# Kernel tuning notes

Hardware: AMD Instinct MI355X
Metric: run time of the kernel (lower is better)

Reference implementation:

```python
import jax, jax.numpy as jnp
import numpy as np

WS = 7            # small window size
WU = 14           # big window size (2*WS)
DIM = 192
HEADS = 6
HD = DIM // HEADS
HID = int(DIM * 4.0)

def _rel_index():
    bc = np.stack(np.meshgrid(np.arange(WU), np.arange(WU), indexing='ij')).reshape(2, -1)
    sc = np.stack(np.meshgrid(np.arange(WS), np.arange(WS), indexing='ij')).reshape(2, -1)
    rc = (bc[:, :, None] - sc[:, None, :]).transpose(1, 2, 0).astype(np.int64)  # [196,49,2]
    rc[..., 0] += WU - 1
    rc[..., 1] += WU - 1
    rc[..., 0] *= 2 * WU - 1
    return rc.sum(-1)  # [196,49]

REL_IDX = jnp.asarray(_rel_index())

def _layernorm(x, w, b):
    mu = x.mean(-1, keepdims=True)
    var = ((x - mu) ** 2).mean(-1, keepdims=True)
    return (x - mu) * jax.lax.rsqrt(var + 1e-5) * w + b

def _partition(x, ws):
    # x: (B,H,W,C) -> (B*nW, ws*ws, C)
    B, H, W, C = x.shape
    x = x.reshape(B, H // ws, ws, W // ws, ws, C).transpose(0, 1, 3, 2, 4, 5)
    return x.reshape(-1, ws * ws, C)

def _reverse(win, ws, B, H, W):
    C = win.shape[-1]
    x = win.reshape(B, H // ws, W // ws, ws, ws, C).transpose(0, 1, 3, 2, 4, 5)
    return x.reshape(B, H, W, C)

def setup_inputs() -> dict:
    key = jax.random.key(0)
    ks = jax.random.split(key, 12)
    s = 0.02
    return {
        'big_x': jax.random.normal(ks[0], (2, DIM, 224, 224), jnp.float32),
        'small_x': jax.random.normal(ks[1], (2, DIM, 112, 112), jnp.float32),
        'norm_w': jnp.ones((DIM,), jnp.float32),
        'norm_b': jnp.zeros((DIM,), jnp.float32),
        'qkv_w': jax.random.normal(ks[2], (DIM, 3 * DIM), jnp.float32) * s,
        'qkv_b': jnp.zeros((3 * DIM,), jnp.float32),
        'rpb_table': jax.random.normal(ks[3], ((2 * WU - 1) ** 2, HEADS), jnp.float32) * s,
        'proj_w': jax.random.normal(ks[4], (DIM, DIM), jnp.float32) * s,
        'proj_b': jnp.zeros((DIM,), jnp.float32),
        'fc1_w': jax.random.normal(ks[5], (DIM, HID), jnp.float32) * s,
        'fc1_b': jnp.zeros((HID,), jnp.float32),
        'fc2_w': jax.random.normal(ks[6], (HID, DIM), jnp.float32) * s,
        'fc2_b': jnp.zeros((DIM,), jnp.float32),
    }

def reference(big_x, small_x, norm_w, norm_b, qkv_w, qkv_b, rpb_table,
              proj_w, proj_b, fc1_w, fc1_b, fc2_w, fc2_b):
    B, C, Hb, Wb = big_x.shape
    shortcut = big_x.transpose(0, 2, 3, 1)              # B,H,W,C
    bx = _layernorm(shortcut, norm_w, norm_b)
    sx = _layernorm(small_x.transpose(0, 2, 3, 1), norm_w, norm_b)

    xb = _partition(bx, WU)                             # (Bw, 196, C)
    xs = _partition(sx, WS)                             # (Bw, 49, C)
    Bw, Nb, _ = xb.shape
    Ns = xs.shape[1]

    def qkv_split(x, N):
        q = (x @ qkv_w + qkv_b).reshape(-1, N, 3, HEADS, HD).transpose(2, 0, 3, 1, 4)
        return q[0], q[1], q[2]

    qb, _, _ = qkv_split(xb, Nb)
    _, ks_, vs = qkv_split(xs, Ns)

    # NOTE: original forward never applies self.scale -> no scaling, faithful.
    attn = jnp.einsum('bhnd,bhmd->bhnm', qb, ks_)       # (Bw,H,196,49)
    bias = rpb_table[REL_IDX]                           # (196,49,H)
    attn = jax.nn.softmax(attn + bias.transpose(2, 0, 1)[None], axis=-1)
    out = jnp.einsum('bhnm,bhmd->bhnd', attn, vs)       # (Bw,H,196,hd)
    out = out.transpose(0, 2, 1, 3).reshape(Bw, Nb, C)
    out = out @ proj_w + proj_b

    x = shortcut + _reverse(out, WU, B, Hb, Wb)
    h = _layernorm(x, norm_w, norm_b)
    h = jax.nn.gelu(h @ fc1_w + fc1_b, approximate=False) @ fc2_w + fc2_b
    x = x + h
    return x.transpose(0, 3, 1, 2)
```

## Files before the change

### kernel.cpp

```cpp
#include <hip/hip_runtime.h>
#include <hip/hip_bf16.h>

typedef __attribute__((ext_vector_type(8))) short bf16x8;
typedef __attribute__((ext_vector_type(4))) float f32x4;

__device__ __forceinline__ unsigned short f2b(float f){
  union { float f; unsigned int u; } v; v.f = f;
  unsigned int r = (v.u + 0x7FFFu + ((v.u >> 16) & 1u)) >> 16;
  return (unsigned short)r;
}
__device__ __forceinline__ float b2f(unsigned short s){
  union { unsigned int u; float f; } v; v.u = ((unsigned int)s) << 16;
  return v.f;
}
__device__ __forceinline__ f32x4 mfma16(bf16x8 a, bf16x8 b, f32x4 c){
  return __builtin_amdgcn_mfma_f32_16x16x32_bf16(a, b, c, 0, 0, 0);
}


__global__ __launch_bounds__(256) void k_wconv(const float* __restrict__ qkv_w, const float* __restrict__ proj_w,
                                               const float* __restrict__ fc1_w, const float* __restrict__ fc2_w,
                                               unsigned short* __restrict__ wT){
  int i = blockIdx.x*256 + threadIdx.x;
  if (i < 110592){
    int k = i / 576, n = i - k*576;
    wT[n*192 + k] = f2b(qkv_w[i]);
  } else if (i < 147456){
    int j = i - 110592; int k = j / 192, n = j - k*192;
    wT[110592 + n*192 + k] = f2b(proj_w[j]);
  } else if (i < 294912){
    int j = i - 147456; int k = j / 768, n = j - k*768;
    wT[147456 + n*192 + k] = f2b(fc1_w[j]);
  } else {
    int j = i - 294912; int k = j / 192, n = j - k*192;
    wT[294912 + n*768 + k] = f2b(fc2_w[j]);
  }
}

template<int IMG, int WSZ, int NTOK>
__global__ __launch_bounds__(256) void k_ln(const float* __restrict__ xin, const float* __restrict__ nw,
                                            const float* __restrict__ nb, unsigned short* __restrict__ out){
  const int HW = IMG*IMG;
  int tid = threadIdx.x;
  int p = blockIdx.x*256 + tid;
  int b = p / HW, rem = p - b*HW;
  const float* base = xin + (size_t)b*192*HW + rem;
  float s = 0.f, s2 = 0.f;
  for (int c = 0; c < 192; c++){ float v = base[(size_t)c*HW]; s += v; s2 += v*v; }
  float mu = s*(1.f/192.f);
  float var = s2*(1.f/192.f) - mu*mu;
  float rs = rsqrtf(var + 1e-5f);
  int y = rem / IMG, xx = rem - y*IMG;
  int wy = y / WSZ, iy = y - wy*WSZ, wx = xx / WSZ, ix = xx - wx*WSZ;
  int t = ((b*16 + wy)*16 + wx)*NTOK + iy*WSZ + ix;
  __shared__ int srow[256];
  __shared__ unsigned short tile[256][66];
  srow[tid] = t*192;
  int lane = tid & 63, w = tid >> 6;
  for (int c0 = 0; c0 < 192; c0 += 64){
    for (int j = 0; j < 64; j++){
      int c = c0 + j;
      float v = base[(size_t)c*HW];
      tile[tid][j] = f2b((v - mu)*rs*nw[c] + nb[c]);
    }
    __syncthreads();
    for (int i = 0; i < 64; i++){
      int pix = w*64 + i;
      out[srow[pix] + c0 + lane] = tile[pix][lane];
    }
    __syncthreads();
  }
}

__global__ __launch_bounds__(256) void k_gemm_full(const unsigned short* A, const unsigned short* Bt,
                                                   const float* __restrict__ bias, unsigned short* C, int Nstride){
  int m0 = blockIdx.x * 64;
  int nbase = blockIdx.y * 192;
  int tid = threadIdx.x, lane = tid & 63, w = tid >> 6;
  int wm = w & 1, wn = w >> 1;
  int r16 = lane & 15, g = lane >> 4, kk8 = g*8;
  __shared__ __align__(16) unsigned short Al[64][40];
  __shared__ __align__(16) unsigned short Bl[192][40];
  f32x4 acc[2][6];
  const f32x4 zz = {0.f,0.f,0.f,0.f};
  for (int a_ = 0; a_ < 2; a_++) for (int b_ = 0; b_ < 6; b_++) acc[a_][b_] = zz;
  int srow = tid >> 2, sseg = (tid & 3)*8;
  for (int k0 = 0; k0 < 192; k0 += 32){
    *(bf16x8*)&Al[srow][sseg] = *(const bf16x8*)&A[(size_t)(m0 + srow)*192 + k0 + sseg];
    for (int s = 0; s < 3; s++){
      int rr = srow + 64*s;
      *(bf16x8*)&Bl[rr][sseg] = *(const bf16x8*)&Bt[(size_t)(nbase + rr)*192 + k0 + sseg];
    }
    __syncthreads();
    bf16x8 a0 = *(bf16x8*)&Al[wm*32 + r16][kk8];
    bf16x8 a1 = *(bf16x8*)&Al[wm*32 + 16 + r16][kk8];
    for (int nj = 0; nj < 6; nj++){
      bf16x8 bb = *(bf16x8*)&Bl[wn*96 + nj*16 + r16][kk8];
      acc[0][nj] = mfma16(a0, bb, acc[0][nj]);
      acc[1][nj] = mfma16(a1, bb, acc[1][nj]);
    }
    __syncthreads();
  }
  for (int mi = 0; mi < 2; mi++) for (int nj = 0; nj < 6; nj++){
    int n = wn*96 + nj*16 + r16;
    float bv = bias[nbase + n];
    for (int r = 0; r < 4; r++){
      int m = m0 + wm*32 + mi*16 + g*4 + r;
      C[(size_t)m*Nstride + nbase + n] = f2b(acc[mi][nj][r] + bv);
    }
  }
}

__global__ __launch_bounds__(256) void k_proj_res(const unsigned short* __restrict__ A,
                                                  const unsigned short* __restrict__ Bt,
                                                  const float* __restrict__ bias,
                                                  const float* __restrict__ big, float* __restrict__ xout){
  int pix0 = blockIdx.x * 64;
  int b = pix0 / 50176, rem0 = pix0 - b*50176;
  int tid = threadIdx.x, lane = tid & 63, w = tid >> 6;
  int wm = w & 1, wn = w >> 1;
  int r16 = lane & 15, g = lane >> 4, kk8 = g*8;
  __shared__ int tok[64];
  __shared__ __align__(16) char smem[49664];
  unsigned short (*Al)[40] = (unsigned short (*)[40])smem;
  unsigned short (*Bl)[40] = (unsigned short (*)[40])(smem + 5120);
  float (*ot)[193] = (float (*)[193])smem;
  if (tid < 64){
    int rem = rem0 + tid, y = rem / 224, x = rem - y*224;
    tok[tid] = ((b*16 + y/14)*16 + x/14)*196 + (y%14)*14 + (x%14);
  }
  __syncthreads();
  int srow = tid >> 2, sseg = (tid & 3)*8;
  int myTok = tok[srow];
  f32x4 acc[2][6];
  const f32x4 zz = {0.f,0.f,0.f,0.f};
  for (int a_ = 0; a_ < 2; a_++) for (int b_ = 0; b_ < 6; b_++) acc[a_][b_] = zz;
  for (int k0 = 0; k0 < 192; k0 += 32){
    *(bf16x8*)&Al[srow][sseg] = *(const bf16x8*)&A[(size_t)myTok*192 + k0 + sseg];
    for (int s = 0; s < 3; s++){
      int rr = srow + 64*s;
      *(bf16x8*)&Bl[rr][sseg] = *(const bf16x8*)&Bt[(size_t)rr*192 + k0 + sseg];
    }
    __syncthreads();
    bf16x8 a0 = *(bf16x8*)&Al[wm*32 + r16][kk8];
    bf16x8 a1 = *(bf16x8*)&Al[wm*32 + 16 + r16][kk8];
    for (int nj = 0; nj < 6; nj++){
      bf16x8 bb = *(bf16x8*)&Bl[wn*96 + nj*16 + r16][kk8];
      acc[0][nj] = mfma16(a0, bb, acc[0][nj]);
      acc[1][nj] = mfma16(a1, bb, acc[1][nj]);
    }
    __syncthreads();
  }
  for (int mi = 0; mi < 2; mi++) for (int nj = 0; nj < 6; nj++){
    int n = wn*96 + nj*16 + r16;
    float bv = bias[n];
    for (int r = 0; r < 4; r++)
      ot[wm*32 + mi*16 + g*4 + r][n] = acc[mi][nj][r] + bv;
  }
  __syncthreads();
  for (int j = 0; j < 48; j++){
    int flat = j*256 + tid;
    int c = flat >> 6, p = flat & 63;
    size_t addr = ((size_t)b*192 + c)*50176 + rem0 + p;
    xout[addr] = ot[p][c] + big[addr];
  }
}

__global__ __launch_bounds__(256) void k_attn(unsigned short* q, const unsigned short* __restrict__ kv,
                                              const float* __restrict__ rpb){
  int win = blockIdx.x / 6, head = blockIdx.x - win*6;
  int tid = threadIdx.x, lane = tid & 63, w = tid >> 6;
  __shared__ __align__(16) unsigned short ql[208][40];
  __shared__ __align__(16) unsigned short kl[64][40];
  __shared__ __align__(16) unsigned short vt[32][72];
  __shared__ __align__(16) unsigned short plds[4][16][72];
  __shared__ float rb[729];
  float4 z4; z4.x = z4.y = z4.z = z4.w = 0.f;
  {
    float4* a4 = (float4*)&ql[0][0];
    for (int i = tid; i < 1040; i += 256) a4[i] = z4;
    float4* b4 = (float4*)&kl[0][0];
    for (int i = tid; i < 320; i += 256) b4[i] = z4;
    float4* c4 = (float4*)&vt[0][0];
    for (int i = tid; i < 288; i += 256) c4[i] = z4;
  }
  __syncthreads();
  const unsigned short* qbase = q + (size_t)win*196*192 + head*32;
  for (int r4 = tid; r4 < 784; r4 += 256){
    int r = r4 >> 2, seg = (r4 & 3)*8;
    *(bf16x8*)&ql[r][seg] = *(const bf16x8*)&qbase[(size_t)r*192 + seg];
  }
  const unsigned short* kbase = kv + (size_t)win*49*384 + head*32;
  if (tid < 196){
    int r = tid >> 2, seg = (tid & 3)*8;
    *(bf16x8*)&kl[r][seg] = *(const bf16x8*)&kbase[(size_t)r*384 + seg];
  }
  const unsigned short* vbase = kbase + 192;
  for (int md = tid; md < 392; md += 256){
    int m = md >> 3, d0 = (md & 7)*4;
    const unsigned short* src = vbase + (size_t)m*384 + d0;
    vt[d0][m] = src[0]; vt[d0+1][m] = src[1]; vt[d0+2][m] = src[2]; vt[d0+3][m] = src[3];
  }
  for (int i = tid; i < 729; i += 256) rb[i] = rpb[i*6 + head];
  __syncthreads();
  int r16 = lane & 15, g = lane >> 4, kk8 = g*8;
  const f32x4 zz = {0.f,0.f,0.f,0.f};
  unsigned short* obase = q + (size_t)win*196*192 + head*32;
  for (int mt = w; mt < 13; mt += 4){
    bf16x8 a = *(bf16x8*)&ql[mt*16 + r16][kk8];
    f32x4 s[4];
    for (int nt = 0; nt < 4; nt++){
      bf16x8 bb = *(bf16x8*)&kl[nt*16 + r16][kk8];
      s[nt] = mfma16(a, bb, zz);
    }
    int nb0 = mt*16 + g*4;
    for (int nt = 0; nt < 4; nt++){
      int m = nt*16 + r16;
      if (m < 49){
        int jy = m / 7, jx = m - jy*7;
        for (int r = 0; r < 4; r++){
          int n = nb0 + r; if (n > 195) n = 195;
          int iy = n / 14, ix = n - iy*14;
          s[nt][r] += rb[(iy - jy + 13)*27 + (ix - jx + 13)];
        }
      } else {
        s[nt][0] = -1e30f; s[nt][1] = -1e30f; s[nt][2] = -1e30f; s[nt][3] = -1e30f;
      }
    }
    for (int r = 0; r < 4; r++){
      float mx = fmaxf(fmaxf(s[0][r], s[1][r]), fmaxf(s[2][r], s[3][r]));
      mx = fmaxf(mx, __shfl_xor(mx, 1, 16));
      mx = fmaxf(mx, __shfl_xor(mx, 2, 16));
      mx = fmaxf(mx, __shfl_xor(mx, 4, 16));
      mx = fmaxf(mx, __shfl_xor(mx, 8, 16));
      float sum = 0.f;
      for (int nt = 0; nt < 4; nt++){ float e = __expf(s[nt][r] - mx); s[nt][r] = e; sum += e; }
      sum += __shfl_xor(sum, 1, 16);
      sum += __shfl_xor(sum, 2, 16);
      sum += __shfl_xor(sum, 4, 16);
      sum += __shfl_xor(sum, 8, 16);
      float inv = 1.0f / sum;
      for (int nt = 0; nt < 4; nt++) s[nt][r] *= inv;
    }
    for (int nt = 0; nt < 4; nt++)
      for (int r = 0; r < 4; r++)
        plds[w][g*4 + r][nt*16 + r16] = f2b(s[nt][r]);
    asm volatile("s_waitcnt lgkmcnt(0)" ::: "memory");
    f32x4 o0 = zz, o1 = zz;
    for (int ks = 0; ks < 2; ks++){
      bf16x8 pa = *(bf16x8*)&plds[w][r16][ks*32 + kk8];
      bf16x8 v0 = *(bf16x8*)&vt[r16][ks*32 + kk8];
      bf16x8 v1 = *(bf16x8*)&vt[16 + r16][ks*32 + kk8];
      o0 = mfma16(pa, v0, o0);
      o1 = mfma16(pa, v1, o1);
    }
    for (int r = 0; r < 4; r++){
      int n = nb0 + r;
      if (n < 196){
        obase[(size_t)n*192 + r16]      = f2b(o0[r]);
        obase[(size_t)n*192 + 16 + r16] = f2b(o1[r]);
      }
    }
  }
}

__global__ __launch_bounds__(512) void k_mlp(float* xio, const unsigned short* __restrict__ fc1T, const float* __restrict__ b1,
                                             const unsigned short* __restrict__ fc2T, const float* __restrict__ b2,
                                             const float* __restrict__ nw, const float* __restrict__ nb){
  __shared__ __align__(16) unsigned short xv[64][198];
  __shared__ __align__(16) unsigned short xln[64][200];
  __shared__ __align__(16) unsigned short ul[64][72];
  int pix0 = blockIdx.x * 64;
  int b = pix0 / 50176, rem0 = pix0 - b*50176;
  int tid = threadIdx.x, lane = tid & 63, w = tid >> 6;
  float xr[24];
  for (int i = 0; i < 24; i++){
    int c = i*8 + (tid >> 6), p = tid & 63;
    float v = xio[((size_t)b*192 + c)*50176 + rem0 + p];
    xr[i] = v;
    xv[p][c] = f2b(v);
  }
  __syncthreads();
  {
    int row = tid >> 3, sub = tid & 7;
    float s = 0.f, s2 = 0.f;
    for (int j = 0; j < 24; j++){ float v = b2f(xv[row][sub*24 + j]); s += v; s2 += v*v; }
    s  += __shfl_xor(s, 1, 8);  s2 += __shfl_xor(s2, 1, 8);
    s  += __shfl_xor(s, 2, 8);  s2 += __shfl_xor(s2, 2, 8);
    s  += __shfl_xor(s, 4, 8);  s2 += __shfl_xor(s2, 4, 8);
    float mu = s*(1.f/192.f), var = s2*(1.f/192.f) - mu*mu, rs = rsqrtf(var + 1e-5f);
    for (int j = 0; j < 24; j++){
      int c = sub*24 + j;
      float v = b2f(xv[row][c]);
      xln[row][c] = f2b((v - mu)*rs*nw[c] + nb[c]);
    }
  }
  __syncthreads();
  int wm = w >> 2, wn = w & 3;
  int r16 = lane & 15, g = lane >> 4, kk8 = g*8;
  const f32x4 zz = {0.f,0.f,0.f,0.f};
  f32x4 acc2[2][3];
  acc2[0][0]=zz; acc2[0][1]=zz; acc2[0][2]=zz; acc2[1][0]=zz; acc2[1][1]=zz; acc2[1][2]=zz;
  for (int kh = 0; kh < 12; kh++){
    f32x4 u0 = zz, u1 = zz;
    int nc = kh*64 + wn*16 + r16;
    for (int ks = 0; ks < 6; ks++){
      bf16x8 bb = *(const bf16x8*)&fc1T[(size_t)nc*192 + ks*32 + kk8];
      bf16x8 a0 = *(bf16x8*)&xln[wm*32 + r16][ks*32 + kk8];
      bf16x8 a1 = *(bf16x8*)&xln[wm*32 + 16 + r16][ks*32 + kk8];
      u0 = mfma16(a0, bb, u0);
      u1 = mfma16(a1, bb, u1);
    }
    float bias1 = b1[nc];
    for (int r = 0; r < 4; r++){
      float uu = u0[r] + bias1;
      ul[wm*32 + g*4 + r][wn*16 + r16]      = f2b(0.5f*uu*(1.f + erff(uu*0.70710678f)));
      float vv = u1[r] + bias1;
      ul[wm*32 + 16 + g*4 + r][wn*16 + r16] = f2b(0.5f*vv*(1.f + erff(vv*0.70710678f)));
    }
    __syncthreads();
    for (int ks = 0; ks < 2; ks++){
      bf16x8 a0 = *(bf16x8*)&ul[wm*32 + r16][ks*32 + kk8];
      bf16x8 a1 = *(bf16x8*)&ul[wm*32 + 16 + r16][ks*32 + kk8];
      for (int j = 0; j < 3; j++){
        int n2 = wn*16 + j*64 + r16;
        bf16x8 bb = *(const bf16x8*)&fc2T[(size_t)n2*768 + kh*64 + ks*32 + kk8];
        acc2[0][j] = mfma16(a0, bb, acc2[0][j]);
        acc2[1][j] = mfma16(a1, bb, acc2[1][j]);
      }
    }
    __syncthreads();
  }
  for (int mi = 0; mi < 2; mi++) for (int j = 0; j < 3; j++){
    int c = wn*16 + j*64 + r16;
    float bias2 = b2[c];
    for (int r = 0; r < 4; r++){
      int t = wm*32 + mi*16 + g*4 + r;
      xv[t][c] = f2b(acc2[mi][j][r] + bias2);
    }
  }
  __syncthreads();
  for (int i = 0; i < 24; i++){
    int c = i*8 + (tid >> 6), p = tid & 63;
    xio[((size_t)b*192 + c)*50176 + rem0 + p] = xr[i] + b2f(xv[p][c]);
  }
}

extern "C" void kernel_launch(void* const* d_in, const int* in_sizes, int n_in,
                              void* d_out, int out_size, void* d_ws, size_t ws_size,
                              hipStream_t stream){
  (void)in_sizes; (void)n_in; (void)out_size; (void)ws_size;
  const float* bigx   = (const float*)d_in[0];
  const float* smx    = (const float*)d_in[1];
  const float* nw     = (const float*)d_in[2];
  const float* nb_    = (const float*)d_in[3];
  const float* qkv_w  = (const float*)d_in[4];
  const float* qkv_b  = (const float*)d_in[5];
  const float* rpb    = (const float*)d_in[6];
  const float* proj_w = (const float*)d_in[7];
  const float* proj_b = (const float*)d_in[8];
  const float* fc1_w  = (const float*)d_in[9];
  const float* fc1_b  = (const float*)d_in[10];
  const float* fc2_w  = (const float*)d_in[11];
  const float* fc2_b  = (const float*)d_in[12];

  char* ws = (char*)d_ws;
  unsigned short* wT  = (unsigned short*)ws;
  unsigned short* bxn = (unsigned short*)(ws + 884736);
  unsigned short* xsn = (unsigned short*)(ws + 39419904);
  unsigned short* kvb = (unsigned short*)(ws + 49053696);
  float* xo = (float*)d_out;

  k_wconv<<<1728, 256, 0, stream>>>(qkv_w, proj_w, fc1_w, fc2_w, wT);
  k_ln<224,14,196><<<392, 256, 0, stream>>>(bigx, nw, nb_, bxn);
  k_ln<112,7,49><<<98, 256, 0, stream>>>(smx, nw, nb_, xsn);
  k_gemm_full<<<dim3(1568,1), 256, 0, stream>>>(bxn, wT, qkv_b, bxn, 192);
  k_gemm_full<<<dim3(392,2), 256, 0, stream>>>(xsn, wT + 36864, qkv_b + 192, kvb, 384);
  k_attn<<<3072, 256, 0, stream>>>(bxn, kvb, rpb);
  k_proj_res<<<1568, 256, 0, stream>>>(bxn, wT + 110592, proj_b, bigx, xo);
  k_mlp<<<1568, 512, 0, stream>>>(xo, wT + 147456, fc1_b, wT + 294912, fc2_b, nw, nb_);
}
```

Measured before the change: 684.3 us.

## Double-buffer MLP hidden chunks, drop register/LDS copies, raise occupancy

Restructures k_mlp so the next fc1+GELU chunk is computed into a second LDS buffer while the current chunk feeds fc2, removing one barrier per iteration. The fc1 K-loop is split into two independent accumulator chains for more MFMA ILP. The layernorm output overwrites the input buffer and the 24-float residual register copy is dropped, with the residual re-read from global at the end. A min-blocks hint of 5 is added to launch_bounds to lower register and LDS pressure for higher occupancy. The trade is an extra global read of x and possible register spills under the tighter bound.

```diff
diff --git a/kernel.cpp b/kernel.cpp
--- a/kernel.cpp
+++ b/kernel.cpp
@@ -264,21 +264,17 @@
   }
 }
 
-__global__ __launch_bounds__(512) void k_mlp(float* xio, const unsigned short* __restrict__ fc1T, const float* __restrict__ b1,
-                                             const unsigned short* __restrict__ fc2T, const float* __restrict__ b2,
-                                             const float* __restrict__ nw, const float* __restrict__ nb){
-  __shared__ __align__(16) unsigned short xv[64][198];
-  __shared__ __align__(16) unsigned short xln[64][200];
-  __shared__ __align__(16) unsigned short ul[64][72];
+__global__ __launch_bounds__(512, 5) void k_mlp(float* xio, const unsigned short* __restrict__ fc1T, const float* __restrict__ b1,
+                                                const unsigned short* __restrict__ fc2T, const float* __restrict__ b2,
+                                                const float* __restrict__ nw, const float* __restrict__ nb){
+  __shared__ __align__(16) unsigned short xv[64][200];
+  __shared__ __align__(16) unsigned short ul[2][64][72];
   int pix0 = blockIdx.x * 64;
   int b = pix0 / 50176, rem0 = pix0 - b*50176;
   int tid = threadIdx.x, lane = tid & 63, w = tid >> 6;
-  float xr[24];
   for (int i = 0; i < 24; i++){
     int c = i*8 + (tid >> 6), p = tid & 63;
-    float v = xio[((size_t)b*192 + c)*50176 + rem0 + p];
-    xr[i] = v;
-    xv[p][c] = f2b(v);
+    xv[p][c] = f2b(xio[((size_t)b*192 + c)*50176 + rem0 + p]);
   }
   __syncthreads();
   {
@@ -292,36 +288,47 @@
     for (int j = 0; j < 24; j++){
       int c = sub*24 + j;
       float v = b2f(xv[row][c]);
-      xln[row][c] = f2b((v - mu)*rs*nw[c] + nb[c]);
+      xv[row][c] = f2b((v - mu)*rs*nw[c] + nb[c]);
     }
   }
   __syncthreads();
   int wm = w >> 2, wn = w & 3;
   int r16 = lane & 15, g = lane >> 4, kk8 = g*8;
   const f32x4 zz = {0.f,0.f,0.f,0.f};
+
+#define FC1_CHUNK(KH, BUF)                                                          \
+  {                                                                                 \
+    f32x4 u0a = zz, u0b = zz, u1a = zz, u1b = zz;                                   \
+    int nc = (KH)*64 + wn*16 + r16;                                                 \
+    for (int ks = 0; ks < 3; ks++){                                                 \
+      bf16x8 bb0 = *(const bf16x8*)&fc1T[(size_t)nc*192 + ks*32 + kk8];             \
+      bf16x8 bb1 = *(const bf16x8*)&fc1T[(size_t)nc*192 + (ks+3)*32 + kk8];         \
+      bf16x8 a0 = *(bf16x8*)&xv[wm*32 + r16][ks*32 + kk8];                          \
+      bf16x8 a1 = *(bf16x8*)&xv[wm*32 + 16 + r16][ks*32 + kk8];                     \
+      bf16x8 a0b = *(bf16x8*)&xv[wm*32 + r16][(ks+3)*32 + kk8];                     \
+      bf16x8 a1b = *(bf16x8*)&xv[wm*32 + 16 + r16][(ks+3)*32 + kk8];                \
+      u0a = mfma16(a0, bb0, u0a);  u1a = mfma16(a1, bb0, u1a);                      \
+      u0b = mfma16(a0b, bb1, u0b); u1b = mfma16(a1b, bb1, u1b);                     \
+    }                                                                               \
+    float b1v = b1[nc];                                                             \
+    for (int r = 0; r < 4; r++){                                                    \
+      float uu = u0a[r] + u0b[r] + b1v;                                             \
+      ul[BUF][wm*32 + g*4 + r][wn*16 + r16]      = f2b(0.5f*uu*(1.f + erff(uu*0.70710678f))); \
+      float vv = u1a[r] + u1b[r] + b1v;                                             \
+      ul[BUF][wm*32 + 16 + g*4 + r][wn*16 + r16] = f2b(0.5f*vv*(1.f + erff(vv*0.70710678f))); \
+    }                                                                               \
+  }
+
   f32x4 acc2[2][3];
   acc2[0][0]=zz; acc2[0][1]=zz; acc2[0][2]=zz; acc2[1][0]=zz; acc2[1][1]=zz; acc2[1][2]=zz;
+  FC1_CHUNK(0, 0)
+  __syncthreads();
   for (int kh = 0; kh < 12; kh++){
-    f32x4 u0 = zz, u1 = zz;
-    int nc = kh*64 + wn*16 + r16;
-    for (int ks = 0; ks < 6; ks++){
-      bf16x8 bb = *(const bf16x8*)&fc1T[(size_t)nc*192 + ks*32 + kk8];
-      bf16x8 a0 = *(bf16x8*)&xln[wm*32 + r16][ks*32 + kk8];
-      bf16x8 a1 = *(bf16x8*)&xln[wm*32 + 16 + r16][ks*32 + kk8];
-      u0 = mfma16(a0, bb, u0);
-      u1 = mfma16(a1, bb, u1);
-    }
-    float bias1 = b1[nc];
-    for (int r = 0; r < 4; r++){
-      float uu = u0[r] + bias1;
-      ul[wm*32 + g*4 + r][wn*16 + r16]      = f2b(0.5f*uu*(1.f + erff(uu*0.70710678f)));
-      float vv = u1[r] + bias1;
-      ul[wm*32 + 16 + g*4 + r][wn*16 + r16] = f2b(0.5f*vv*(1.f + erff(vv*0.70710678f)));
-    }
-    __syncthreads();
+    int cur = kh & 1;
+    if (kh < 11){ FC1_CHUNK(kh+1, cur^1) }
     for (int ks = 0; ks < 2; ks++){
-      bf16x8 a0 = *(bf16x8*)&ul[wm*32 + r16][ks*32 + kk8];
-      bf16x8 a1 = *(bf16x8*)&ul[wm*32 + 16 + r16][ks*32 + kk8];
+      bf16x8 a0 = *(bf16x8*)&ul[cur][wm*32 + r16][ks*32 + kk8];
+      bf16x8 a1 = *(bf16x8*)&ul[cur][wm*32 + 16 + r16][ks*32 + kk8];
       for (int j = 0; j < 3; j++){
         int n2 = wn*16 + j*64 + r16;
         bf16x8 bb = *(const bf16x8*)&fc2T[(size_t)n2*768 + kh*64 + ks*32 + kk8];
@@ -331,6 +338,7 @@
     }
     __syncthreads();
   }
+#undef FC1_CHUNK
   for (int mi = 0; mi < 2; mi++) for (int j = 0; j < 3; j++){
     int c = wn*16 + j*64 + r16;
     float bias2 = b2[c];
@@ -342,7 +350,8 @@
   __syncthreads();
   for (int i = 0; i < 24; i++){
     int c = i*8 + (tid >> 6), p = tid & 63;
-    xio[((size_t)b*192 + c)*50176 + rem0 + p] = xr[i] + b2f(xv[p][c]);
+    size_t addr = ((size_t)b*192 + c)*50176 + rem0 + p;
+    xio[addr] = xio[addr] + b2f(xv[p][c]);
   }
 }
 
```

Measured after the change: 668.9 us. 1.02x faster.
